# Optimization experiments

Measured on AMD Instinct MI355X. Metric: run time of the kernel, lower is better.

Reference implementation:

```python
import jax, jax.numpy as jnp
import numpy as np

B, S, H, NCOL, NH = 32, 512, 768, 32, 12
HD = H // NH  # head dim 64
LN_EPS = 1e-12


def setup_inputs() -> dict:
    key = jax.random.key(0)
    ks = jax.random.split(key, 20)
    s = 0.02
    inp = {
        'hidden_states': jax.random.normal(ks[0], (B, S, H), jnp.float32),
        'column_embeddings': jax.random.normal(ks[1], (B, NCOL, H), jnp.float32),
        'column_categories': jax.random.randint(ks[2], (B, NCOL), 0, 2, jnp.int32),
        'value_mask': jax.random.randint(ks[3], (B, S), 0, NCOL + 1, jnp.int32),
        'Wd': jax.random.normal(ks[4], (H, H), jnp.float32) * s,
        'bd': jnp.zeros((H,), jnp.float32),
        'Wc': jax.random.normal(ks[5], (H, H), jnp.float32) * s,
        'bc': jnp.zeros((H,), jnp.float32),
        'Wq': jax.random.normal(ks[6], (H, H), jnp.float32) * s,
        'bq': jnp.zeros((H,), jnp.float32),
        'Wk': jax.random.normal(ks[7], (H, H), jnp.float32) * s,
        'bk': jnp.zeros((H,), jnp.float32),
        'Wv': jax.random.normal(ks[8], (H, H), jnp.float32) * s,
        'bv': jnp.zeros((H,), jnp.float32),
        'Wo': jax.random.normal(ks[9], (H, H), jnp.float32) * s,
        'bo': jnp.zeros((H,), jnp.float32),
        'ln_g': jnp.ones((H,), jnp.float32),
        'ln_b': jnp.zeros((H,), jnp.float32),
    }
    return inp


def _layernorm(x, g, b):
    mu = jnp.mean(x, axis=-1, keepdims=True)
    var = jnp.mean(jnp.square(x - mu), axis=-1, keepdims=True)
    return (x - mu) * jax.lax.rsqrt(var + LN_EPS) * g + b


def reference(hidden_states, column_embeddings, column_categories, value_mask,
              Wd, bd, Wc, bc, Wq, bq, Wk, bk, Wv, bv, Wo, bo, ln_g, ln_b):
    # dense branch
    h_ = hidden_states @ Wd.T + bd  # [B,S,H]
    # column gather: zero out category==0 columns, prepend zero row for index 0
    table = column_embeddings * (column_categories == 1)[..., None].astype(column_embeddings.dtype)
    table = jnp.concatenate([jnp.zeros_like(table[:, :1]), table], axis=1)  # [B,NCOL+1,H]
    h_col = jnp.take_along_axis(table, value_mask[..., None].astype(jnp.int32), axis=1)  # [B,S,H]
    h = jax.nn.gelu(h_ + (h_col @ Wc.T + bc), approximate=False)
    # Roberta self-attention
    def heads(x):
        return x.reshape(B, S, NH, HD).transpose(0, 2, 1, 3)  # [B,NH,S,HD]
    q = heads(h @ Wq.T + bq)
    k = heads(h @ Wk.T + bk)
    v = heads(h @ Wv.T + bv)
    scores = jnp.einsum('bhsd,bhtd->bhst', q, k) / jnp.sqrt(jnp.float32(HD))
    probs = jax.nn.softmax(scores, axis=-1)
    ctx = jnp.einsum('bhst,bhtd->bhsd', probs, v).transpose(0, 2, 1, 3).reshape(B, S, H)
    # self-output: dense + residual + layernorm
    out = _layernorm(ctx @ Wo.T + bo + h, ln_g, ln_b)
    return out
```

## Files before the change

### kernel.cpp

```cpp
#include <hip/hip_runtime.h>
#include <hip/hip_bf16.h>
#include <math.h>
#include <stdint.h>

#define B_    32
#define S_    512
#define H_    768
#define NH_   12
#define HD_   64
#define NCOL_ 32
#define M_    (B_*S_)

typedef __bf16 bf16;
typedef __bf16 bf16x8 __attribute__((ext_vector_type(8)));
typedef __bf16 bf16x4 __attribute__((ext_vector_type(4)));
typedef float  f32x4  __attribute__((ext_vector_type(4)));

__device__ __forceinline__ void async_load16(const void* g, void* l) {
    __builtin_amdgcn_global_load_lds(
        (__attribute__((address_space(1))) unsigned int*)g,
        (__attribute__((address_space(3))) unsigned int*)l, 16, 0, 0);
}

__device__ __forceinline__ bf16x8 cvt8(const float* p) {
    const float4* fp = (const float4*)p;
    float4 x = fp[0], y = fp[1];
    bf16x8 r;
    r[0] = (bf16)x.x; r[1] = (bf16)x.y; r[2] = (bf16)x.z; r[3] = (bf16)x.w;
    r[4] = (bf16)y.x; r[5] = (bf16)y.y; r[6] = (bf16)y.z; r[7] = (bf16)y.w;
    return r;
}

__global__ __launch_bounds__(256) void cvt_kernel(
    const float* __restrict__ hidden, const float* __restrict__ ce,
    const int* __restrict__ cc, const int* __restrict__ vm,
    const float* __restrict__ Wd, const float* __restrict__ Wc,
    const float* __restrict__ Wq, const float* __restrict__ Wk,
    const float* __restrict__ Wv, const float* __restrict__ Wo,
    const float* __restrict__ bq, const float* __restrict__ bk,
    const float* __restrict__ bv,
    bf16* __restrict__ hbf, bf16* __restrict__ hcol,
    bf16* __restrict__ wpack, float* __restrict__ bqkv)
{
    int blk = blockIdx.x;
    if (blk < 6144) {
        int id = blk * 256 + threadIdx.x;
        int row = id / 96, c = id - row * 96;
        *(bf16x8*)&hbf[(long)row * H_ + c * 8] = cvt8(hidden + (long)row * H_ + c * 8);
    } else if (blk < 12288) {
        int id = (blk - 6144) * 256 + threadIdx.x;
        int row = id / 96, c = id - row * 96;
        int b = row >> 9;
        int m = vm[row];
        bf16x8 val;
#pragma unroll
        for (int i = 0; i < 8; i++) val[i] = (bf16)0.0f;
        if (m > 0) {
            int col = m - 1;
            if (cc[b * NCOL_ + col] == 1)
                val = cvt8(ce + ((long)(b * NCOL_ + col)) * H_ + c * 8);
        }
        *(bf16x8*)&hcol[(long)row * H_ + c * 8] = val;
    } else {
        int id = (blk - 12288) * 256 + threadIdx.x;
        if (id < 442368) {
            const float* src;
            int r = id;
            if      (r < 73728)  { src = Wd; }
            else if (r < 147456) { src = Wc; r -= 73728; }
            else if (r < 221184) { src = Wq; r -= 147456; }
            else if (r < 294912) { src = Wk; r -= 221184; }
            else if (r < 368640) { src = Wv; r -= 294912; }
            else                 { src = Wo; r -= 368640; }
            *(bf16x8*)&wpack[(long)id * 8] = cvt8(src + (long)r * 8);
        } else if (id < 442656) {
            int j0 = (id - 442368) * 8;
#pragma unroll
            for (int i = 0; i < 8; i++) {
                int j = j0 + i;
                float v = (j < 768) ? bq[j] : (j < 1536) ? bk[j - 768] : bv[j - 1536];
                bqkv[j] = v;
            }
        }
    }
}

__global__ __launch_bounds__(512, 4) void gemm_qkv(
    const bf16* __restrict__ A, const bf16* __restrict__ Bw,
    const float* __restrict__ bias, bf16* __restrict__ out)
{
    __shared__ __align__(16) bf16 LB[36864];

    const int tid  = threadIdx.x;
    const int lane = tid & 63;
    const int wave = tid >> 6;
    const int wr   = wave >> 1;
    const int wc   = wave & 1;
    const int quad = lane >> 4;
    const int ln16 = lane & 15;
    const int m0   = blockIdx.x * 256;
    const int n0   = blockIdx.y * 128;

    int arow[2], acol[2];
#pragma unroll
    for (int q = 0; q < 2; q++) {
        int l = q * 512 + tid;
        int row = l >> 2;
        arow[q] = row;
        acol[q] = ((l & 3) ^ ((row >> 1) & 3)) * 8;
    }
    const int brow = tid >> 2;
    const int bcol = ((tid & 3) ^ ((brow >> 1) & 3)) * 8;

    auto stage = [&](int kt, int bsel) {
        int kk = kt * 32;
        const bf16* ag = A + kk;
        const bf16* bg = Bw + kk;
        bf16* SAb = &LB[bsel * 8192];
        bf16* SBb = &LB[24576 + bsel * 4096];
        async_load16(ag + (long)(m0 + arow[0]) * H_ + acol[0], SAb + tid * 8);
        async_load16(ag + (long)(m0 + arow[1]) * H_ + acol[1], SAb + 4096 + tid * 8);
        async_load16(bg + (long)(n0 + brow)    * H_ + bcol,    SBb + tid * 8);
    };

    f32x4 acc[4][4];
    const f32x4 zero4 = {0.f, 0.f, 0.f, 0.f};
#pragma unroll
    for (int i = 0; i < 4; i++)
#pragma unroll
        for (int j = 0; j < 4; j++) acc[i][j] = zero4;

    const int s4 = (ln16 >> 1) & 3;
    int aoff[4], boff[4];
#pragma unroll
    for (int i = 0; i < 4; i++) {
        aoff[i] = (wr * 64 + i * 16 + ln16) * 32 + (quad ^ s4) * 8;
        boff[i] = (wc * 64 + i * 16 + ln16) * 32 + (quad ^ s4) * 8;
    }

    const int nt = 24;

    stage(0, 0);
    stage(1, 1);
    asm volatile("s_waitcnt vmcnt(3)" ::: "memory");
    __builtin_amdgcn_sched_barrier(0);
    __builtin_amdgcn_s_barrier();

    int bs = 0;
    for (int t = 0; t < nt; ++t) {
        const int ps = (bs + 2 >= 3) ? bs - 1 : bs + 2;

        bf16x8 af[4], bfr[4];
#pragma unroll
        for (int i = 0; i < 4; i++) af[i]  = *(const bf16x8*)&LB[bs * 8192 + aoff[i]];
#pragma unroll
        for (int j = 0; j < 4; j++) bfr[j] = *(const bf16x8*)&LB[24576 + bs * 4096 + boff[j]];
        if (t + 2 < nt) stage(t + 2, ps);

        __builtin_amdgcn_s_setprio(1);
#pragma unroll
        for (int i = 0; i < 4; i++)
#pragma unroll
            for (int j = 0; j < 4; j++)
                acc[i][j] = __builtin_amdgcn_mfma_f32_16x16x32_bf16(af[i], bfr[j], acc[i][j], 0, 0, 0);
        __builtin_amdgcn_s_setprio(0);

        if (t + 2 < nt)       { asm volatile("s_waitcnt vmcnt(3)" ::: "memory"); }
        else if (t + 1 < nt)  { asm volatile("s_waitcnt vmcnt(0)" ::: "memory"); }
        __builtin_amdgcn_sched_barrier(0);
        if (t + 1 < nt) __builtin_amdgcn_s_barrier();
        bs = (bs + 1 == 3) ? 0 : bs + 1;
    }

    __syncthreads();
    bf16* scr = &LB[wave * 4608];

    const int cs0  = n0 + wc * 64;
    const int sec  = (cs0 >= 1536) ? 2 : ((cs0 >= 768) ? 1 : 0);
    const int head = (cs0 - sec * 768) >> 6;
    bf16* dst = out + (long)sec * M_ * H_;

#pragma unroll
    for (int j = 0; j < 4; j++) {
        const int d_loc = j * 16 + ln16;
        const float bj = bias[cs0 + d_loc];
#pragma unroll
        for (int i = 0; i < 4; i++) {
#pragma unroll
            for (int r = 0; r < 4; r++) {
                const int s_loc = i * 16 + quad * 4 + r;
                const float v = acc[i][j][r] + bj;
                scr[(sec == 2) ? (d_loc * 72 + s_loc) : (s_loc * 72 + d_loc)] = (bf16)v;
            }
        }
    }
    asm volatile("s_waitcnt lgkmcnt(0)" ::: "memory");
    __builtin_amdgcn_sched_barrier(0);

    const int g8 = lane >> 3;
    const int o8 = (lane & 7) * 8;
    if (sec < 2) {
#pragma unroll
        for (int it = 0; it < 8; it++) {
            const int s_loc = it * 8 + g8;
            const int row_s = m0 + wr * 64 + s_loc;
            const int b = row_s >> 9, s = row_s & 511;
            *(bf16x8*)&dst[(((long)(b * NH_ + head)) * S_ + s) * HD_ + o8] =
                *(const bf16x8*)&scr[s_loc * 72 + o8];
        }
    } else {
        const int row0 = m0 + wr * 64;
        const int b = row0 >> 9, sb = row0 & 511;
#pragma unroll
        for (int it = 0; it < 8; it++) {
            const int d_loc = it * 8 + g8;
            *(bf16x8*)&dst[(((long)(b * NH_ + head)) * HD_ + d_loc) * S_ + sb + o8] =
                *(const bf16x8*)&scr[d_loc * 72 + o8];
        }
    }
}

template<int MODE>
__global__ __launch_bounds__(256, 3) void gemm_bt(
    const bf16* __restrict__ A0, const bf16* __restrict__ A1,
    const bf16* __restrict__ B0, const bf16* __restrict__ B1,
    const float* __restrict__ bias1, const float* __restrict__ bias2,
    const bf16* __restrict__ resid, bf16* __restrict__ out,
    int K, int KSPLIT)
{
    __shared__ __align__(16) bf16 SA[3][128 * 32];
    __shared__ __align__(16) bf16 SB[3][128 * 32];

    const int tid  = threadIdx.x;
    const int lane = tid & 63;
    const int wave = tid >> 6;
    const int wr   = wave >> 1;
    const int wc   = wave & 1;
    const int quad = lane >> 4;
    const int ln16 = lane & 15;
    const int m0   = blockIdx.x * 128;
    const int n0   = blockIdx.y * 128;

    int arow[2], acol[2];
#pragma unroll
    for (int q = 0; q < 2; q++) {
        int l = q * 256 + tid;
        int row = l >> 2;
        arow[q] = row;
        acol[q] = ((l & 3) ^ ((row >> 1) & 3)) * 8;
    }

    auto stage = [&](int kt, int bsel) {
        int kk = kt * 32;
        const bf16* ag = (kk < KSPLIT) ? A0 + kk : A1 + (kk - KSPLIT);
        const bf16* bg = (kk < KSPLIT) ? B0 + kk : B1 + (kk - KSPLIT);
        async_load16(ag + (long)(m0 + arow[0]) * H_ + acol[0], &SA[bsel][tid * 8]);
        async_load16(ag + (long)(m0 + arow[1]) * H_ + acol[1], &SA[bsel][2048 + tid * 8]);
        async_load16(bg + (long)(n0 + arow[0]) * H_ + acol[0], &SB[bsel][tid * 8]);
        async_load16(bg + (long)(n0 + arow[1]) * H_ + acol[1], &SB[bsel][2048 + tid * 8]);
    };

    f32x4 acc[4][4];
    const f32x4 zero4 = {0.f, 0.f, 0.f, 0.f};
#pragma unroll
    for (int i = 0; i < 4; i++)
#pragma unroll
        for (int j = 0; j < 4; j++) acc[i][j] = zero4;

    const int s4 = (ln16 >> 1) & 3;
    int aoff[4], boff[4];
#pragma unroll
    for (int i = 0; i < 4; i++) {
        aoff[i] = (wr * 64 + i * 16 + ln16) * 32 + (quad ^ s4) * 8;
        boff[i] = (wc * 64 + i * 16 + ln16) * 32 + (quad ^ s4) * 8;
    }

    const int nt = K >> 5;

    stage(0, 0);
    stage(1, 1);
    asm volatile("s_waitcnt vmcnt(4)" ::: "memory");
    __builtin_amdgcn_sched_barrier(0);
    __builtin_amdgcn_s_barrier();

    int bs = 0;
    for (int t = 0; t < nt; ++t) {
        const int ps = (bs + 2 >= 3) ? bs - 1 : bs + 2;

        bf16x8 af[4], bfr[4];
#pragma unroll
        for (int i = 0; i < 4; i++) af[i]  = *(const bf16x8*)&SA[bs][aoff[i]];
#pragma unroll
        for (int j = 0; j < 4; j++) bfr[j] = *(const bf16x8*)&SB[bs][boff[j]];
        if (t + 2 < nt) stage(t + 2, ps);

        __builtin_amdgcn_s_setprio(1);
#pragma unroll
        for (int i = 0; i < 4; i++)
#pragma unroll
            for (int j = 0; j < 4; j++)
                acc[i][j] = __builtin_amdgcn_mfma_f32_16x16x32_bf16(af[i], bfr[j], acc[i][j], 0, 0, 0);
        __builtin_amdgcn_s_setprio(0);

        if (t + 2 < nt)       { asm volatile("s_waitcnt vmcnt(4)" ::: "memory"); }
        else if (t + 1 < nt)  { asm volatile("s_waitcnt vmcnt(0)" ::: "memory"); }
        __builtin_amdgcn_sched_barrier(0);
        if (t + 1 < nt) __builtin_amdgcn_s_barrier();
        bs = (bs + 1 == 3) ? 0 : bs + 1;
    }

    const int c_r = quad * 4;
    const int c_c = ln16;

#pragma unroll
    for (int j = 0; j < 4; j++) {
        const int col = n0 + wc * 64 + j * 16 + c_c;
        float bias = bias1[col];
        if (MODE == 0) bias += bias2[col];
#pragma unroll
        for (int i = 0; i < 4; i++) {
#pragma unroll
            for (int r = 0; r < 4; r++) {
                const int row = m0 + wr * 64 + i * 16 + c_r + r;
                float v = acc[i][j][r] + bias;
                if (MODE == 0) {
                    v = 0.5f * v * (1.0f + erff(v * 0.70710678118654752f));
                    out[(long)row * H_ + col] = (bf16)v;
                } else {
                    v += (float)resid[(long)row * H_ + col];
                    out[(long)row * H_ + col] = (bf16)v;
                }
            }
        }
    }
}

#define QP 72

__global__ __launch_bounds__(256) void attn_kernel(
    const bf16* __restrict__ q, const bf16* __restrict__ k,
    const bf16* __restrict__ vt, bf16* __restrict__ ctx)
{
    __shared__ __align__(16) bf16 Qs[64 * QP];
    __shared__ __align__(16) bf16 Ks[64 * QP];
    __shared__ __align__(16) bf16 Vt[64 * QP];
    __shared__ __align__(16) bf16 Ps[4][16 * QP];

    const int tid  = threadIdx.x;
    const int lane = tid & 63;
    const int w    = tid >> 6;
    const int quad = lane >> 4;
    const int ln16 = lane & 15;

    const int bid = blockIdx.x;
    const int qt  = bid / 384;
    const int g   = bid - qt * 384;
    const int b   = g / 12;
    const int h   = g - b * 12;
    const long base = ((long)(b * NH_ + h)) * S_ * HD_;

    const int r0 = tid >> 2;
    const int e0 = (tid & 3) * 16;

    {
        const bf16* qg = q + base + (long)qt * 64 * HD_;
        *(uint4*)&Qs[r0 * QP + e0]     = *(const uint4*)&qg[r0 * HD_ + e0];
        *(uint4*)&Qs[r0 * QP + e0 + 8] = *(const uint4*)&qg[r0 * HD_ + e0 + 8];
    }
    const bf16* kg = k  + base;
    const bf16* vg = vt + base;
    uint4 kr0 = *(const uint4*)&kg[r0 * HD_ + e0];
    uint4 kr1 = *(const uint4*)&kg[r0 * HD_ + e0 + 8];
    uint4 vr0 = *(const uint4*)&vg[(long)r0 * S_ + e0];
    uint4 vr1 = *(const uint4*)&vg[(long)r0 * S_ + e0 + 8];
    __syncthreads();

    const bf16x8 bq0 = *(const bf16x8*)&Qs[(w * 16 + ln16) * QP + quad * 8];
    const bf16x8 bq1 = *(const bf16x8*)&Qs[(w * 16 + ln16) * QP + 32 + quad * 8];

    f32x4 O[4];
    const f32x4 zero4 = {0.f, 0.f, 0.f, 0.f};
#pragma unroll
    for (int t = 0; t < 4; t++) O[t] = zero4;
    float mo = -1e30f, l = 0.f;

    for (int kc = 0; kc < 8; kc++) {
        __syncthreads();
        *(uint4*)&Ks[r0 * QP + e0]     = kr0;
        *(uint4*)&Ks[r0 * QP + e0 + 8] = kr1;
        *(uint4*)&Vt[r0 * QP + e0]     = vr0;
        *(uint4*)&Vt[r0 * QP + e0 + 8] = vr1;
        {
            int kcn = (kc < 7) ? kc + 1 : 7;
            kr0 = *(const uint4*)&kg[(long)kcn * 64 * HD_ + r0 * HD_ + e0];
            kr1 = *(const uint4*)&kg[(long)kcn * 64 * HD_ + r0 * HD_ + e0 + 8];
            vr0 = *(const uint4*)&vg[(long)r0 * S_ + kcn * 64 + e0];
            vr1 = *(const uint4*)&vg[(long)r0 * S_ + kcn * 64 + e0 + 8];
        }
        __syncthreads();

        f32x4 sc[4];
#pragma unroll
        for (int i = 0; i < 4; i++) {
            bf16x8 a0 = *(const bf16x8*)&Ks[(i * 16 + ln16) * QP + quad * 8];
            bf16x8 a1 = *(const bf16x8*)&Ks[(i * 16 + ln16) * QP + 32 + quad * 8];
            sc[i] = zero4;
            sc[i] = __builtin_amdgcn_mfma_f32_16x16x32_bf16(a0, bq0, sc[i], 0, 0, 0);
            sc[i] = __builtin_amdgcn_mfma_f32_16x16x32_bf16(a1, bq1, sc[i], 0, 0, 0);
        }

        float cm = -1e30f;
#pragma unroll
        for (int i = 0; i < 4; i++)
#pragma unroll
            for (int r = 0; r < 4; r++) {
                float s = sc[i][r] * 0.125f;
                sc[i][r] = s;
                cm = fmaxf(cm, s);
            }
        cm = fmaxf(cm, __shfl_xor(cm, 16));
        cm = fmaxf(cm, __shfl_xor(cm, 32));
        float mn = fmaxf(mo, cm);
        float alpha = __expf(mo - mn);
        float rs = 0.f;
#pragma unroll
        for (int i = 0; i < 4; i++) {
            bf16x4 pk;
#pragma unroll
            for (int r = 0; r < 4; r++) {
                float p = __expf(sc[i][r] - mn);
                rs += p;
                pk[r] = (bf16)p;
            }
            *(bf16x4*)&Ps[w][ln16 * QP + i * 16 + quad * 4] = pk;
        }
        rs += __shfl_xor(rs, 16);
        rs += __shfl_xor(rs, 32);
        l  = l * alpha + rs;
        mo = mn;
#pragma unroll
        for (int t = 0; t < 4; t++)
#pragma unroll
            for (int r = 0; r < 4; r++) O[t][r] *= alpha;

        bf16x8 bp0 = *(const bf16x8*)&Ps[w][ln16 * QP + quad * 8];
        bf16x8 bp1 = *(const bf16x8*)&Ps[w][ln16 * QP + 32 + quad * 8];
#pragma unroll
        for (int dt = 0; dt < 4; dt++) {
            bf16x8 a0 = *(const bf16x8*)&Vt[(dt * 16 + ln16) * QP + quad * 8];
            bf16x8 a1 = *(const bf16x8*)&Vt[(dt * 16 + ln16) * QP + 32 + quad * 8];
            O[dt] = __builtin_amdgcn_mfma_f32_16x16x32_bf16(a0, bp0, O[dt], 0, 0, 0);
            O[dt] = __builtin_amdgcn_mfma_f32_16x16x32_bf16(a1, bp1, O[dt], 0, 0, 0);
        }
    }

    {
        float inv = 1.0f / l;
#pragma unroll
        for (int dt = 0; dt < 4; dt++) {
            bf16x4 ov;
#pragma unroll
            for (int r = 0; r < 4; r++) ov[r] = (bf16)(O[dt][r] * inv);
            *(bf16x4*)&Qs[(w * 16 + ln16) * QP + dt * 16 + quad * 4] = ov;
        }
    }
    __syncthreads();
    {
        uint4 o0 = *(const uint4*)&Qs[r0 * QP + e0];
        uint4 o1 = *(const uint4*)&Qs[r0 * QP + e0 + 8];
        bf16* cg = ctx + ((long)(b * S_ + qt * 64 + r0)) * H_ + h * HD_;
        *(uint4*)&cg[e0]     = o0;
        *(uint4*)&cg[e0 + 8] = o1;
    }
}

__global__ __launch_bounds__(256) void ln_kernel(
    const bf16* __restrict__ y, const float* __restrict__ g,
    const float* __restrict__ be, float* __restrict__ out)
{
    const int lane = threadIdx.x & 63;
    const int w    = threadIdx.x >> 6;
    const long row = (long)blockIdx.x * 4 + w;
    const bf16* yr = y + row * H_;

    float x[12];
    float sum = 0.f, ss = 0.f;
#pragma unroll
    for (int j = 0; j < 12; j++) {
        x[j] = (float)yr[j * 64 + lane];
        sum += x[j];
        ss  += x[j] * x[j];
    }
#pragma unroll
    for (int m = 1; m < 64; m <<= 1) {
        sum += __shfl_xor(sum, m);
        ss  += __shfl_xor(ss, m);
    }
    const float mu  = sum * (1.0f / 768.0f);
    float var = ss * (1.0f / 768.0f) - mu * mu;
    const float rs = rsqrtf(fmaxf(var, 0.f) + 1e-12f);
#pragma unroll
    for (int j = 0; j < 12; j++) {
        int c = j * 64 + lane;
        out[row * H_ + c] = (x[j] - mu) * rs * g[c] + be[c];
    }
}

extern "C" void kernel_launch(void* const* d_in, const int* in_sizes, int n_in,
                              void* d_out, int out_size, void* d_ws, size_t ws_size,
                              hipStream_t stream)
{
    const float* hidden = (const float*)d_in[0];
    const float* ce     = (const float*)d_in[1];
    const int*   cc     = (const int*)d_in[2];
    const int*   vm     = (const int*)d_in[3];
    const float* Wd     = (const float*)d_in[4];
    const float* bd     = (const float*)d_in[5];
    const float* Wc     = (const float*)d_in[6];
    const float* bc     = (const float*)d_in[7];
    const float* Wq     = (const float*)d_in[8];
    const float* bq     = (const float*)d_in[9];
    const float* Wk     = (const float*)d_in[10];
    const float* bk     = (const float*)d_in[11];
    const float* Wv     = (const float*)d_in[12];
    const float* bv     = (const float*)d_in[13];
    const float* Wo     = (const float*)d_in[14];
    const float* bo     = (const float*)d_in[15];
    const float* lng    = (const float*)d_in[16];
    const float* lnb    = (const float*)d_in[17];

    const long NE = (long)M_ * H_;
    bf16* ws   = (bf16*)d_ws;
    bf16* hbuf = ws;
    bf16* qkv  = ws + NE;
    bf16* hbf  = qkv;
    bf16* hcol = qkv + NE;
    bf16* qb   = qkv;
    bf16* kb   = qkv + NE;
    bf16* vb   = qkv + 2 * NE;
    bf16* wpack = ws + 4 * NE;
    const bf16* Wd_b  = wpack;
    const bf16* Wc_b  = wpack + 589824;
    const bf16* Wq_b  = wpack + 1179648;
    const bf16* Wo_b  = wpack + 2949120;
    float* bqkv = (float*)(wpack + 3538944);
    bf16* ctx = (bf16*)d_out;

    cvt_kernel<<<14018, 256, 0, stream>>>(hidden, ce, cc, vm, Wd, Wc, Wq, Wk, Wv, Wo,
                                          bq, bk, bv, hbf, hcol, wpack, bqkv);

    dim3 g6(M_ / 128, 6);
    gemm_bt<0><<<g6, 256, 0, stream>>>(hbf, hcol, Wd_b, Wc_b, bd, bc, nullptr, hbuf, 2 * H_, H_);
    gemm_qkv<<<dim3(M_ / 256, 18), 512, 0, stream>>>(hbuf, Wq_b, bqkv, qkv);
    attn_kernel<<<3072, 256, 0, stream>>>(qb, kb, vb, ctx);
    gemm_bt<2><<<g6, 256, 0, stream>>>(ctx, ctx, Wo_b, Wo_b, bo, nullptr, hbuf, hbuf, H_, H_);
    ln_kernel<<<M_ / 4, 256, 0, stream>>>(hbuf, lng, lnb, (float*)d_out);
}
```

Baseline: 366.7 us.

## Precompute column-embedding projection table instead of gathering and multiplying per token

Uses linearity: h_col @ Wc^T is a gather from column_embeddings @ Wc^T, so the product is computed once for the 1024 masked column rows (a small GEMM of 48 tiles inside the conversion kernel). The per-token lookup is then added in the first GEMM's epilogue via value_mask. This halves the K dimension of the first GEMM and drops the materialized hcol tensor, at the cost of a scattered fp32 table read per output element and a slow unpipelined mini-GEMM in 48 blocks of the conversion kernel.

After: 391.8 us. 1.07x slower.

```diff
diff --git a/kernel.cpp b/kernel.cpp
--- a/kernel.cpp
+++ b/kernel.cpp
@@ -33,36 +33,101 @@
 
 __global__ __launch_bounds__(256) void cvt_kernel(
     const float* __restrict__ hidden, const float* __restrict__ ce,
-    const int* __restrict__ cc, const int* __restrict__ vm,
+    const int* __restrict__ cc,
     const float* __restrict__ Wd, const float* __restrict__ Wc,
     const float* __restrict__ Wq, const float* __restrict__ Wk,
     const float* __restrict__ Wv, const float* __restrict__ Wo,
     const float* __restrict__ bq, const float* __restrict__ bk,
     const float* __restrict__ bv,
-    bf16* __restrict__ hbf, bf16* __restrict__ hcol,
-    bf16* __restrict__ wpack, float* __restrict__ bqkv)
+    bf16* __restrict__ hbf, bf16* __restrict__ wpack,
+    float* __restrict__ bqkv, float* __restrict__ tableP)
 {
-    int blk = blockIdx.x;
-    if (blk < 6144) {
-        int id = blk * 256 + threadIdx.x;
+    __shared__ __align__(16) bf16 MA[128 * 32];
+    __shared__ __align__(16) bf16 MB[128 * 32];
+
+    const int blk = blockIdx.x;
+    const int tid = threadIdx.x;
+
+    if (blk < 48) {
+        const int mp = blk & 7;
+        const int np = blk >> 3;
+        const int lane = tid & 63, wave = tid >> 6;
+        const int wr = wave >> 1, wc = wave & 1;
+        const int quad = lane >> 4, ln16 = lane & 15;
+        const int s4 = (ln16 >> 1) & 3;
+
+        f32x4 acc[4][4];
+        const f32x4 zero4 = {0.f, 0.f, 0.f, 0.f};
+#pragma unroll
+        for (int i = 0; i < 4; i++)
+#pragma unroll
+            for (int j = 0; j < 4; j++) acc[i][j] = zero4;
+
+        int aoff[4], boff[4];
+#pragma unroll
+        for (int i = 0; i < 4; i++) {
+            aoff[i] = (wr * 64 + i * 16 + ln16) * 32 + (quad ^ s4) * 8;
+            boff[i] = (wc * 64 + i * 16 + ln16) * 32 + (quad ^ s4) * 8;
+        }
+
+        const int l0 = tid, l1 = tid + 256;
+        const int row0 = l0 >> 2, row1 = l1 >> 2;
+        const int cl0 = ((l0 & 3) ^ ((row0 >> 1) & 3)) * 8;
+        const int cl1 = ((l1 & 3) ^ ((row1 >> 1) & 3)) * 8;
+        const int ga0 = mp * 128 + row0, ga1 = mp * 128 + row1;
+        const int gb0 = np * 128 + row0, gb1 = np * 128 + row1;
+        const bool mk0 = (cc[ga0] == 1), mk1 = (cc[ga1] == 1);
+
+        bf16x8 zz;
+#pragma unroll
+        for (int i = 0; i < 8; i++) zz[i] = (bf16)0.0f;
+
+        for (int kt = 0; kt < 24; ++kt) {
+            const int kk = kt * 32;
+            bf16x8 a0 = mk0 ? cvt8(ce + (long)ga0 * H_ + kk + cl0) : zz;
+            bf16x8 a1 = mk1 ? cvt8(ce + (long)ga1 * H_ + kk + cl1) : zz;
+            bf16x8 b0 = cvt8(Wc + (long)gb0 * H_ + kk + cl0);
+            bf16x8 b1 = cvt8(Wc + (long)gb1 * H_ + kk + cl1);
+            __syncthreads();
+            *(bf16x8*)&MA[l0 * 8] = a0;
+            *(bf16x8*)&MA[l1 * 8] = a1;
+            *(bf16x8*)&MB[l0 * 8] = b0;
+            *(bf16x8*)&MB[l1 * 8] = b1;
+            __syncthreads();
+
+            bf16x8 af[4], bfr[4];
+#pragma unroll
+            for (int i = 0; i < 4; i++) af[i]  = *(const bf16x8*)&MA[aoff[i]];
+#pragma unroll
+            for (int j = 0; j < 4; j++) bfr[j] = *(const bf16x8*)&MB[boff[j]];
+#pragma unroll
+            for (int i = 0; i < 4; i++)
+#pragma unroll
+                for (int j = 0; j < 4; j++)
+                    acc[i][j] = __builtin_amdgcn_mfma_f32_16x16x32_bf16(af[i], bfr[j], acc[i][j], 0, 0, 0);
+        }
+
+        const int c_r = quad * 4;
+#pragma unroll
+        for (int j = 0; j < 4; j++) {
+            const int col = np * 128 + wc * 64 + j * 16 + ln16;
+#pragma unroll
+            for (int i = 0; i < 4; i++)
+#pragma unroll
+                for (int r = 0; r < 4; r++) {
+                    const int row = mp * 128 + wr * 64 + i * 16 + c_r + r;
+                    tableP[(long)row * H_ + col] = acc[i][j][r];
+                }
+        }
+        return;
+    }
+
+    if (blk < 6192) {
+        int id = (blk - 48) * 256 + tid;
         int row = id / 96, c = id - row * 96;
         *(bf16x8*)&hbf[(long)row * H_ + c * 8] = cvt8(hidden + (long)row * H_ + c * 8);
-    } else if (blk < 12288) {
-        int id = (blk - 6144) * 256 + threadIdx.x;
-        int row = id / 96, c = id - row * 96;
-        int b = row >> 9;
-        int m = vm[row];
-        bf16x8 val;
-#pragma unroll
-        for (int i = 0; i < 8; i++) val[i] = (bf16)0.0f;
-        if (m > 0) {
-            int col = m - 1;
-            if (cc[b * NCOL_ + col] == 1)
-                val = cvt8(ce + ((long)(b * NCOL_ + col)) * H_ + c * 8);
-        }
-        *(bf16x8*)&hcol[(long)row * H_ + c * 8] = val;
     } else {
-        int id = (blk - 12288) * 256 + threadIdx.x;
+        int id = (blk - 6192) * 256 + tid;
         if (id < 442368) {
             const float* src;
             int r = id;
@@ -225,8 +290,9 @@
     const bf16* __restrict__ A0, const bf16* __restrict__ A1,
     const bf16* __restrict__ B0, const bf16* __restrict__ B1,
     const float* __restrict__ bias1, const float* __restrict__ bias2,
-    const bf16* __restrict__ resid, bf16* __restrict__ out,
-    int K, int KSPLIT)
+    const bf16* __restrict__ resid,
+    const int* __restrict__ vmk, const float* __restrict__ tp,
+    bf16* __restrict__ out, int K, int KSPLIT)
 {
     __shared__ __align__(16) bf16 SA[3][128 * 32];
     __shared__ __align__(16) bf16 SB[3][128 * 32];
@@ -312,6 +378,18 @@
     const int c_r = quad * 4;
     const int c_c = ln16;
 
+    int tpo[4][4];
+    if (MODE == 0) {
+#pragma unroll
+        for (int i = 0; i < 4; i++)
+#pragma unroll
+            for (int r = 0; r < 4; r++) {
+                const int row = m0 + wr * 64 + i * 16 + c_r + r;
+                const int m = vmk[row];
+                tpo[i][r] = (m > 0) ? ((row >> 9) * NCOL_ + m - 1) * H_ : -1;
+            }
+    }
+
 #pragma unroll
     for (int j = 0; j < 4; j++) {
         const int col = n0 + wc * 64 + j * 16 + c_c;
@@ -324,6 +402,7 @@
                 const int row = m0 + wr * 64 + i * 16 + c_r + r;
                 float v = acc[i][j][r] + bias;
                 if (MODE == 0) {
+                    if (tpo[i][r] >= 0) v += tp[tpo[i][r] + col];
                     v = 0.5f * v * (1.0f + erff(v * 0.70710678118654752f));
                     out[(long)row * H_ + col] = (bf16)v;
                 } else {
@@ -534,25 +613,26 @@
     bf16* hbuf = ws;
     bf16* qkv  = ws + NE;
     bf16* hbf  = qkv;
-    bf16* hcol = qkv + NE;
+    float* tableP = (float*)(qkv + NE);
     bf16* qb   = qkv;
     bf16* kb   = qkv + NE;
     bf16* vb   = qkv + 2 * NE;
     bf16* wpack = ws + 4 * NE;
     const bf16* Wd_b  = wpack;
-    const bf16* Wc_b  = wpack + 589824;
     const bf16* Wq_b  = wpack + 1179648;
     const bf16* Wo_b  = wpack + 2949120;
     float* bqkv = (float*)(wpack + 3538944);
     bf16* ctx = (bf16*)d_out;
 
-    cvt_kernel<<<14018, 256, 0, stream>>>(hidden, ce, cc, vm, Wd, Wc, Wq, Wk, Wv, Wo,
-                                          bq, bk, bv, hbf, hcol, wpack, bqkv);
+    cvt_kernel<<<7922, 256, 0, stream>>>(hidden, ce, cc, Wd, Wc, Wq, Wk, Wv, Wo,
+                                         bq, bk, bv, hbf, wpack, bqkv, tableP);
 
     dim3 g6(M_ / 128, 6);
-    gemm_bt<0><<<g6, 256, 0, stream>>>(hbf, hcol, Wd_b, Wc_b, bd, bc, nullptr, hbuf, 2 * H_, H_);
+    gemm_bt<0><<<g6, 256, 0, stream>>>(hbf, hbf, Wd_b, Wd_b, bd, bc, nullptr,
+                                       vm, tableP, hbuf, H_, H_);
     gemm_qkv<<<dim3(M_ / 256, 18), 512, 0, stream>>>(hbuf, Wq_b, bqkv, qkv);
     attn_kernel<<<3072, 256, 0, stream>>>(qb, kb, vb, ctx);
-    gemm_bt<2><<<g6, 256, 0, stream>>>(ctx, ctx, Wo_b, Wo_b, bo, nullptr, hbuf, hbuf, H_, H_);
+    gemm_bt<2><<<g6, 256, 0, stream>>>(ctx, ctx, Wo_b, Wo_b, bo, nullptr, hbuf,
+                                       nullptr, nullptr, hbuf, H_, H_);
     ln_kernel<<<M_ / 4, 256, 0, stream>>>(hbuf, lng, lnb, (float*)d_out);
 }
```
